# Optimization experiments

Hardware: AMD Instinct MI355X
Metric: run time of the kernel (lower is better)

## Reference

```python
import jax, jax.numpy as jnp
import numpy as np

D = 768          # wav2vec2-base hidden size
H = 4            # cross-attn heads
HD = D // H
B = 8
N = 1024         # w2v sequence length (target length)
T = 2000         # raw CQCC frames
N_GAT = 3
NUM_CLASSES = 2


def _p(key, shape, scale=0.02):
    return jax.random.normal(key, shape, dtype=jnp.float32) * scale


def layer_norm(x, g, b, eps=1e-5):
    m = x.mean(-1, keepdims=True)
    v = x.var(-1, keepdims=True)
    return (x - m) * jax.lax.rsqrt(v + eps) * g + b


def gelu(x):
    return jax.nn.gelu(x, approximate=False)


def conv1d(x, w, b):
    # x [B,C,T], w [O,I,K], padding=1 (same)
    y = jax.lax.conv_general_dilated(x, w, (1,), [(1, 1)], dimension_numbers=('NCH', 'OIH', 'NCH'))
    return y + b[None, :, None]


def batchnorm(x, g, b, m, v, eps=1e-5):
    # eval-mode BatchNorm1d on [B,C,T]
    return (x - m[None, :, None]) * jax.lax.rsqrt(v[None, :, None] + eps) * g[None, :, None] + b[None, :, None]


def interp_linear(x, target_len):
    # torch F.interpolate(mode='linear', align_corners=False); x [B,T,D] -> [B,target_len,D]
    t_in = x.shape[1]
    pos = (jnp.arange(target_len, dtype=jnp.float32) + 0.5) * (t_in / target_len) - 0.5
    pos = jnp.clip(pos, 0.0, t_in - 1.0)
    lo = jnp.floor(pos).astype(jnp.int32)
    hi = jnp.minimum(lo + 1, t_in - 1)
    w = (pos - lo.astype(jnp.float32))[None, :, None]
    return x[:, lo] * (1.0 - w) + x[:, hi] * w


def mha(q, k, v, in_w, in_b, out_w, out_b):
    # torch nn.MultiheadAttention, batch_first=True
    bb, nq, _ = q.shape
    nk = k.shape[1]
    wq, wk, wv = in_w[:D], in_w[D:2 * D], in_w[2 * D:]
    bq, bk, bv = in_b[:D], in_b[D:2 * D], in_b[2 * D:]
    qh = (q @ wq.T + bq).reshape(bb, nq, H, HD).transpose(0, 2, 1, 3)
    kh = (k @ wk.T + bk).reshape(bb, nk, H, HD).transpose(0, 2, 1, 3)
    vh = (v @ wv.T + bv).reshape(bb, nk, H, HD).transpose(0, 2, 1, 3)
    scores = jnp.einsum('bhqd,bhkd->bhqk', qh, kh) * (1.0 / np.sqrt(HD))
    alpha = jax.nn.softmax(scores, axis=-1)
    o = jnp.einsum('bhqk,bhkd->bhqd', alpha, vh).transpose(0, 2, 1, 3).reshape(bb, nq, D)
    return o @ out_w.T + out_b


def graph_attn(x, fc_w, fc_b, a_w, a_b):
    # GAT score on concat([h_i, h_j]) decomposes additively: e_ij = a_i.h_i + a_j.h_j + b
    h = x @ fc_w.T + fc_b                      # [B,N,D]
    s_i = h @ a_w[:D]                          # [B,N]
    s_j = h @ a_w[D:]                          # [B,N]
    e = s_i[:, :, None] + s_j[:, None, :] + a_b  # [B,N,N]
    alpha = jax.nn.softmax(e, axis=-1)
    return jnp.einsum('bij,bjd->bid', alpha, h)


def _forward(w2v, cqcc, conv1_w, conv1_b, bn1_g, bn1_b, bn1_m, bn1_v,
             conv2_w, conv2_b, bn2_g, bn2_b, bn2_m, bn2_v, pos_embed,
             lnq_g, lnq_b, lnkv_g, lnkv_b,
             a1_in_w, a1_in_b, a1_out_w, a1_out_b,
             a2_in_w, a2_in_b, a2_out_w, a2_out_b,
             gat_fc_w, gat_fc_b, gat_a_w, gat_a_b, gln_g, gln_b,
             clf_w1, clf_b1, clf_w2, clf_b2):
    # CQCC conv stack
    x = gelu(batchnorm(conv1d(cqcc, conv1_w, conv1_b), bn1_g, bn1_b, bn1_m, bn1_v))
    x = gelu(batchnorm(conv1d(x, conv2_w, conv2_b), bn2_g, bn2_b, bn2_m, bn2_v))  # [B,D,T]
    cq = interp_linear(x.transpose(0, 2, 1), w2v.shape[1])  # [B,N,D]
    # shared positional encoding
    n = w2v.shape[1]
    w = w2v + pos_embed[:, :n]
    cq = cq + pos_embed[:, :n]
    # bidirectional cross attention (norm_q / norm_kv shared across directions)
    out1 = mha(layer_norm(cq, lnq_g, lnq_b), layer_norm(w, lnkv_g, lnkv_b),
               layer_norm(w, lnkv_g, lnkv_b), a1_in_w, a1_in_b, a1_out_w, a1_out_b)
    out2 = mha(layer_norm(w, lnq_g, lnq_b), layer_norm(cq, lnkv_g, lnkv_b),
               layer_norm(cq, lnkv_g, lnkv_b), a2_in_w, a2_in_b, a2_out_w, a2_out_b)
    x = out1 + out2
    # 3 residual graph-attention blocks
    for l in range(N_GAT):
        res = x
        x = graph_attn(x, gat_fc_w[l], gat_fc_b[l], gat_a_w[l], gat_a_b[l])
        x = layer_norm(x + res, gln_g[l], gln_b[l])
    pooled = x.mean(axis=1)
    h = gelu(pooled @ clf_w1.T + clf_b1)
    return h @ clf_w2.T + clf_b2


def setup_inputs():
    ks = iter(jax.random.split(jax.random.key(0), 64))
    inp = {}
    inp['w2v'] = jax.random.normal(next(ks), (B, N, D), dtype=jnp.float32)
    inp['cqcc'] = jax.random.normal(next(ks), (B, 20, T), dtype=jnp.float32)
    inp['conv1_w'] = _p(next(ks), (128, 20, 3)); inp['conv1_b'] = jnp.zeros((128,), jnp.float32)
    inp['bn1_g'] = jnp.ones((128,), jnp.float32); inp['bn1_b'] = jnp.zeros((128,), jnp.float32)
    inp['bn1_m'] = jnp.zeros((128,), jnp.float32); inp['bn1_v'] = jnp.ones((128,), jnp.float32)
    inp['conv2_w'] = _p(next(ks), (D, 128, 3)); inp['conv2_b'] = jnp.zeros((D,), jnp.float32)
    inp['bn2_g'] = jnp.ones((D,), jnp.float32); inp['bn2_b'] = jnp.zeros((D,), jnp.float32)
    inp['bn2_m'] = jnp.zeros((D,), jnp.float32); inp['bn2_v'] = jnp.ones((D,), jnp.float32)
    inp['pos_embed'] = _p(next(ks), (1, 2000, D), 1.0)
    inp['lnq_g'] = jnp.ones((D,), jnp.float32); inp['lnq_b'] = jnp.zeros((D,), jnp.float32)
    inp['lnkv_g'] = jnp.ones((D,), jnp.float32); inp['lnkv_b'] = jnp.zeros((D,), jnp.float32)
    inp['a1_in_w'] = _p(next(ks), (3 * D, D)); inp['a1_in_b'] = jnp.zeros((3 * D,), jnp.float32)
    inp['a1_out_w'] = _p(next(ks), (D, D)); inp['a1_out_b'] = jnp.zeros((D,), jnp.float32)
    inp['a2_in_w'] = _p(next(ks), (3 * D, D)); inp['a2_in_b'] = jnp.zeros((3 * D,), jnp.float32)
    inp['a2_out_w'] = _p(next(ks), (D, D)); inp['a2_out_b'] = jnp.zeros((D,), jnp.float32)
    inp['gat_fc_w'] = _p(next(ks), (N_GAT, D, D)); inp['gat_fc_b'] = jnp.zeros((N_GAT, D), jnp.float32)
    inp['gat_a_w'] = _p(next(ks), (N_GAT, 2 * D)); inp['gat_a_b'] = jnp.zeros((N_GAT,), jnp.float32)
    inp['gln_g'] = jnp.ones((N_GAT, D), jnp.float32); inp['gln_b'] = jnp.zeros((N_GAT, D), jnp.float32)
    inp['clf_w1'] = _p(next(ks), (128, D)); inp['clf_b1'] = jnp.zeros((128,), jnp.float32)
    inp['clf_w2'] = _p(next(ks), (NUM_CLASSES, 128)); inp['clf_b2'] = jnp.zeros((NUM_CLASSES,), jnp.float32)
    return inp


def reference(w2v, cqcc, conv1_w, conv1_b, bn1_g, bn1_b, bn1_m, bn1_v,
              conv2_w, conv2_b, bn2_g, bn2_b, bn2_m, bn2_v, pos_embed,
              lnq_g, lnq_b, lnkv_g, lnkv_b,
              a1_in_w, a1_in_b, a1_out_w, a1_out_b,
              a2_in_w, a2_in_b, a2_out_w, a2_out_b,
              gat_fc_w, gat_fc_b, gat_a_w, gat_a_b, gln_g, gln_b,
              clf_w1, clf_b1, clf_w2, clf_b2):
    return _forward(w2v, cqcc, conv1_w, conv1_b, bn1_g, bn1_b, bn1_m, bn1_v,
                    conv2_w, conv2_b, bn2_g, bn2_b, bn2_m, bn2_v, pos_embed,
                    lnq_g, lnq_b, lnkv_g, lnkv_b,
                    a1_in_w, a1_in_b, a1_out_w, a1_out_b,
                    a2_in_w, a2_in_b, a2_out_w, a2_out_b,
                    gat_fc_w, gat_fc_b, gat_a_w, gat_a_b, gln_g, gln_b,
                    clf_w1, clf_b1, clf_w2, clf_b2)
```

## Files before the change

### kernel.cpp

```cpp
#include <hip/hip_runtime.h>
#include <math.h>

#define DD 768
#define NH 4
#define HDIM 192
#define BBATCH 8
#define NSEQ 1024
#define TLEN 2000
#define SLOT 6291456

typedef _Float16 h16;
typedef _Float16 half8v __attribute__((ext_vector_type(8)));
typedef _Float16 half4v __attribute__((ext_vector_type(4)));
typedef float f32x4 __attribute__((ext_vector_type(4)));

__device__ __forceinline__ float gelu_f(float x){
  return 0.5f * x * (1.0f + erff(x * 0.70710678118654752440f));
}
__device__ __forceinline__ float wave_sum(float v){
  #pragma unroll
  for (int off = 32; off; off >>= 1) v += __shfl_xor(v, off);
  return v;
}
__device__ __forceinline__ float wave_max(float v){
  #pragma unroll
  for (int off = 32; off; off >>= 1) v = fmaxf(v, __shfl_xor(v, off));
  return v;
}
__device__ __forceinline__ void gload16(const h16* g, h16* l){
  __builtin_amdgcn_global_load_lds(
      (const __attribute__((address_space(1))) void*)g,
      (__attribute__((address_space(3))) void*)l, 16, 0, 0);
}
__device__ __forceinline__ int xcd_remap(int orig, int nwg){
  int q = nwg >> 3, r = nwg & 7;
  int xcd = orig & 7, idx = orig >> 3;
  return (xcd < r ? xcd * (q + 1) : r * (q + 1) + (xcd - r) * q) + idx;
}

__global__ __launch_bounds__(256) void k_cast(const float* __restrict__ s,
    h16* __restrict__ d, int n){
  int i = blockIdx.x * 256 + threadIdx.x;
  if (i < n) d[i] = (h16)s[i];
}

__global__ __launch_bounds__(256) void k_conv1t(const float* __restrict__ cqcc,
    const float* __restrict__ w, const float* __restrict__ bias,
    const float* __restrict__ g, const float* __restrict__ be,
    const float* __restrict__ mm, const float* __restrict__ vv,
    float* __restrict__ out){
  __shared__ float xs[20][258];
  __shared__ float wsm[32*60];
  const int t0 = blockIdx.x * 256;
  const int ocg = blockIdx.y, b = blockIdx.z;
  const int tid = threadIdx.x;
  for (int idx = tid; idx < 20*258; idx += 256){
    int ic = idx / 258, tt = idx % 258;
    int t = t0 + tt - 1;
    xs[ic][tt] = (t >= 0 && t < TLEN) ? cqcc[((size_t)b*20 + ic)*TLEN + t] : 0.f;
  }
  for (int idx = tid; idx < 32*60; idx += 256)
    wsm[idx] = w[ocg*32*60 + idx];
  __syncthreads();
  int t = t0 + tid;
  if (t >= TLEN) return;
  float acc[32] = {};
  for (int ic = 0; ic < 20; ++ic){
    float x0 = xs[ic][tid], x1v = xs[ic][tid+1], x2v = xs[ic][tid+2];
    #pragma unroll
    for (int oc = 0; oc < 32; ++oc){
      const float* wp = &wsm[(oc*20 + ic)*3];
      acc[oc] += wp[0]*x0 + wp[1]*x1v + wp[2]*x2v;
    }
  }
  #pragma unroll 4
  for (int oc = 0; oc < 32; ++oc){
    int c = ocg*32 + oc;
    float s = rsqrtf(vv[c] + 1e-5f) * g[c];
    float val = (acc[oc] + bias[c] - mm[c]) * s + be[c];
    out[((size_t)b*128 + c)*TLEN + t] = gelu_f(val);
  }
}

__global__ __launch_bounds__(256) void k_im2col(const float* __restrict__ x1,
    h16* __restrict__ A2){
  int idx = blockIdx.x * 256 + threadIdx.x;
  if (idx >= 16000*384) return;
  int c = idx % 384, m = idx / 384;
  int b = m / TLEN, t = m % TLEN;
  int ic = c / 3, kh = c % 3;
  int ts = t + kh - 1;
  float v = (ts < 0 || ts >= TLEN) ? 0.f : x1[((size_t)b*128 + ic)*TLEN + ts];
  A2[idx] = (h16)v;
}

__global__ void k_bnprep(const float* __restrict__ cb, const float* __restrict__ g,
    const float* __restrict__ be, const float* __restrict__ m,
    const float* __restrict__ v, float* __restrict__ sc, float* __restrict__ off){
  int i = blockIdx.x * 256 + threadIdx.x;
  if (i >= DD) return;
  float s = g[i] * rsqrtf(v[i] + 1e-5f);
  sc[i] = s;
  off[i] = (cb[i] - m[i]) * s + be[i];
}

__global__ __launch_bounds__(256) void k_interp_ln(const float* __restrict__ x2,
    const float* __restrict__ pe,
    const float* __restrict__ g1, const float* __restrict__ b1, h16* __restrict__ o1,
    const float* __restrict__ g2, const float* __restrict__ b2, h16* __restrict__ o2){
  __shared__ float ss[4], sqq[4];
  int row = blockIdx.x, tid = threadIdx.x;
  int b = row >> 10, i = row & 1023;
  float p = (i + 0.5f) * ((float)TLEN / (float)NSEQ) - 0.5f;
  p = fminf(fmaxf(p, 0.f), (float)(TLEN - 1));
  int lo = (int)floorf(p);
  int hi = min(lo + 1, TLEN - 1);
  float w = p - (float)lo;
  const float* blo = x2 + ((size_t)b * TLEN + lo) * DD;
  const float* bhi = x2 + ((size_t)b * TLEN + hi) * DD;
  const float* per = pe + (size_t)i * DD;
  float v[3]; float s = 0.f, sq = 0.f;
  #pragma unroll
  for (int j = 0; j < 3; ++j){
    int d = j * 256 + tid;
    float x = blo[d] * (1.f - w) + bhi[d] * w + per[d];
    v[j] = x; s += x; sq += x * x;
  }
  s = wave_sum(s); sq = wave_sum(sq);
  int wv = tid >> 6;
  if ((tid & 63) == 0){ ss[wv] = s; sqq[wv] = sq; }
  __syncthreads();
  s  = ss[0] + ss[1] + ss[2] + ss[3];
  sq = sqq[0] + sqq[1] + sqq[2] + sqq[3];
  float mean = s * (1.f / DD);
  float var  = sq * (1.f / DD) - mean * mean;
  float r = rsqrtf(var + 1e-5f);
  #pragma unroll
  for (int j = 0; j < 3; ++j){
    int d = j * 256 + tid;
    float xn = (v[j] - mean) * r;
    o1[(size_t)row * DD + d] = (h16)(xn * g1[d] + b1[d]);
    o2[(size_t)row * DD + d] = (h16)(xn * g2[d] + b2[d]);
  }
}

__global__ __launch_bounds__(256) void k_addpos_ln(const float* __restrict__ xin,
    const float* __restrict__ pe,
    const float* __restrict__ g1, const float* __restrict__ b1, h16* __restrict__ o1,
    const float* __restrict__ g2, const float* __restrict__ b2, h16* __restrict__ o2){
  __shared__ float ss[4], sqq[4];
  int row = blockIdx.x, tid = threadIdx.x;
  int i = row & 1023;
  const float* ip = xin + (size_t)row * DD;
  const float* per = pe + (size_t)i * DD;
  float v[3]; float s = 0.f, sq = 0.f;
  #pragma unroll
  for (int j = 0; j < 3; ++j){
    int d = j * 256 + tid;
    float x = ip[d] + per[d];
    v[j] = x; s += x; sq += x * x;
  }
  s = wave_sum(s); sq = wave_sum(sq);
  int wv = tid >> 6;
  if ((tid & 63) == 0){ ss[wv] = s; sqq[wv] = sq; }
  __syncthreads();
  s  = ss[0] + ss[1] + ss[2] + ss[3];
  sq = sqq[0] + sqq[1] + sqq[2] + sqq[3];
  float mean = s * (1.f / DD);
  float var  = sq * (1.f / DD) - mean * mean;
  float r = rsqrtf(var + 1e-5f);
  #pragma unroll
  for (int j = 0; j < 3; ++j){
    int d = j * 256 + tid;
    float xn = (v[j] - mean) * r;
    o1[(size_t)row * DD + d] = (h16)(xn * g1[d] + b1[d]);
    o2[(size_t)row * DD + d] = (h16)(xn * g2[d] + b2[d]);
  }
}

__global__ __launch_bounds__(256) void k_ln2(const float* __restrict__ in,
    const float* __restrict__ ctx, const float* __restrict__ g,
    const float* __restrict__ be, float* __restrict__ outf, h16* __restrict__ outh){
  __shared__ float ss[4], sqq[4];
  int row = blockIdx.x, tid = threadIdx.x;
  const float* ip = in + (size_t)row * DD;
  int b = row >> 10;
  float v[3]; float s = 0.f, sq = 0.f;
  #pragma unroll
  for (int j = 0; j < 3; ++j){
    int d = j * 256 + tid;
    float x = ip[d];
    if (ctx) x += ctx[b * DD + d];
    v[j] = x; s += x; sq += x * x;
  }
  s = wave_sum(s); sq = wave_sum(sq);
  int w = tid >> 6;
  if ((tid & 63) == 0){ ss[w] = s; sqq[w] = sq; }
  __syncthreads();
  s  = ss[0] + ss[1] + ss[2] + ss[3];
  sq = sqq[0] + sqq[1] + sqq[2] + sqq[3];
  float mean = s * (1.f / DD);
  float var  = sq * (1.f / DD) - mean * mean;
  float r = rsqrtf(var + 1e-5f);
  #pragma unroll
  for (int j = 0; j < 3; ++j){
    int d = j * 256 + tid;
    float y = (v[j] - mean) * r * g[d] + be[d];
    if (outf) outf[(size_t)row * DD + d] = y;
    if (outh) outh[(size_t)row * DD + d] = (h16)y;
  }
}

#define GEMM_MAINLOOP(Abase, lda, Wbase, ldw, Kdim)                          \
  auto stage = [&](int buf, int kt){                                         \
    _Pragma("unroll")                                                        \
    for (int i = 0; i < 4; ++i){                                             \
      int p = i*256 + tid; int row = p >> 3; int ch = (p & 7) ^ (row & 7);   \
      gload16(Abase + (size_t)(m0+row)*lda + kt + ch*8, &Als[buf][p*8]);     \
    }                                                                        \
    _Pragma("unroll")                                                        \
    for (int i = 0; i < 4; ++i){                                             \
      int p = i*256 + tid; int row = p >> 3; int ch = (p & 7) ^ (row & 7);   \
      gload16(Wbase + (size_t)(n0+row)*ldw + kt + ch*8, &Bls[buf][p*8]);     \
    }                                                                        \
  };                                                                         \
  stage(0, 0);                                                               \
  const int nk = Kdim >> 6;                                                  \
  for (int t = 0; t < nk; ++t){                                              \
    const int cur = t & 1;                                                   \
    if (t + 1 < nk){                                                         \
      stage(cur ^ 1, (t + 1) << 6);                                          \
      asm volatile("s_waitcnt vmcnt(8)" ::: "memory");                       \
    } else {                                                                 \
      asm volatile("s_waitcnt vmcnt(0)" ::: "memory");                       \
    }                                                                        \
    __builtin_amdgcn_s_barrier();                                            \
    __builtin_amdgcn_sched_barrier(0);                                       \
    __builtin_amdgcn_s_setprio(1);                                           \
    _Pragma("unroll")                                                        \
    for (int kk = 0; kk < 2; ++kk){                                          \
      half8v af[4], bf[4];                                                   \
      _Pragma("unroll")                                                      \
      for (int mi = 0; mi < 4; ++mi){                                        \
        int row = wr*64 + mi*16 + lr;                                        \
        int chp = (kk*4 + lg) ^ (row & 7);                                   \
        af[mi] = *(const half8v*)&Als[cur][row*64 + chp*8];                  \
      }                                                                      \
      _Pragma("unroll")                                                      \
      for (int ni = 0; ni < 4; ++ni){                                        \
        int row = wc*64 + ni*16 + lr;                                        \
        int chp = (kk*4 + lg) ^ (row & 7);                                   \
        bf[ni] = *(const half8v*)&Bls[cur][row*64 + chp*8];                  \
      }                                                                      \
      _Pragma("unroll")                                                      \
      for (int mi = 0; mi < 4; ++mi)                                         \
        _Pragma("unroll")                                                    \
        for (int ni = 0; ni < 4; ++ni)                                       \
          acc[mi][ni] = __builtin_amdgcn_mfma_f32_16x16x32_f16(              \
              af[mi], bf[ni], acc[mi][ni], 0, 0, 0);                         \
    }                                                                        \
    __builtin_amdgcn_s_setprio(0);                                           \
    asm volatile("s_waitcnt lgkmcnt(0)" ::: "memory");                       \
    __builtin_amdgcn_sched_barrier(0);                                       \
    __builtin_amdgcn_s_barrier();                                            \
  }

__global__ __launch_bounds__(256) void k_gemm_h(
    const h16* __restrict__ A, const h16* __restrict__ W,
    int lda, int ldw, int ldc, int K,
    const float* __restrict__ bias, const float* __restrict__ sc,
    const float* __restrict__ off, const h16* __restrict__ addh,
    float* __restrict__ outf, h16* __restrict__ outh)
{
  __shared__ h16 Als[2][128*64];
  __shared__ h16 Bls[2][128*64];
  const int tid = threadIdx.x;
  const int gx = gridDim.x, gy = gridDim.y;
  const int wg = xcd_remap(blockIdx.x + gx * blockIdx.y, gx * gy);
  const int n0 = (wg % gx) * 128, m0 = (wg / gx) * 128;
  const int lane = tid & 63, wid = tid >> 6;
  const int wr = wid >> 1, wc = wid & 1;
  const int lr = lane & 15, lg = lane >> 4;
  f32x4 acc[4][4] = {};
  GEMM_MAINLOOP(A, lda, W, ldw, K)
  #pragma unroll
  for (int mi = 0; mi < 4; ++mi){
    #pragma unroll
    for (int ni = 0; ni < 4; ++ni){
      int col = n0 + wc*64 + ni*16 + lr;
      int rowb = m0 + wr*64 + mi*16 + lg*4;
      float cb = bias ? bias[col] : 0.f;
      #pragma unroll
      for (int r = 0; r < 4; ++r){
        size_t idx = (size_t)(rowb + r) * ldc + col;
        float v = acc[mi][ni][r];
        if (sc){ v = v * sc[col] + off[col]; v = gelu_f(v); }
        else v += cb;
        if (addh) v += (float)addh[idx];
        if (outf) outf[idx] = v;
        if (outh) outh[idx] = (h16)v;
      }
    }
  }
}

__global__ __launch_bounds__(256) void k_gemm6(
    const h16* __restrict__ Lall, const h16* __restrict__ w6,
    const float* __restrict__ b1, const float* __restrict__ b2,
    h16* __restrict__ qkv6)
{
  __shared__ h16 Als[2][128*64];
  __shared__ h16 Bls[2][128*64];
  const int tid = threadIdx.x;
  const int gx = gridDim.x, gy = gridDim.y;
  const int nwg = gx * gy * 6;
  const int wg = xcd_remap(blockIdx.x + gx*(blockIdx.y + gy*blockIdx.z), nwg);
  const int n0 = (wg % gx) * 128;
  const int m0 = ((wg / gx) % gy) * 128;
  const int bz = wg / (gx * gy);
  const int aidx = (1468 >> (2*bz)) & 3;
  const h16* A = Lall + (size_t)aidx * SLOT;
  const h16* W = w6 + (size_t)bz * 589824;
  const float* bias = (bz < 3 ? b1 + bz*DD : b2 + (bz-3)*DD);
  h16* C = qkv6 + (size_t)bz * SLOT;
  const int lane = tid & 63, wid = tid >> 6;
  const int wr = wid >> 1, wc = wid & 1;
  const int lr = lane & 15, lg = lane >> 4;
  f32x4 acc[4][4] = {};
  GEMM_MAINLOOP(A, DD, W, DD, DD)
  #pragma unroll
  for (int mi = 0; mi < 4; ++mi){
    #pragma unroll
    for (int ni = 0; ni < 4; ++ni){
      int col = n0 + wc*64 + ni*16 + lr;
      int rowb = m0 + wr*64 + mi*16 + lg*4;
      float cb = bias[col];
      #pragma unroll
      for (int r = 0; r < 4; ++r)
        C[(size_t)(rowb + r) * DD + col] = (h16)(acc[mi][ni][r] + cb);
    }
  }
}

__global__ __launch_bounds__(256) void k_trV(const h16* __restrict__ Vh, int ldv,
    h16* __restrict__ VT){
  __shared__ h16 tile[32][36];
  const int z = blockIdx.z, b = z >> 2, h = z & 3;
  const int q0 = blockIdx.x * 32, d0 = blockIdx.y * 32;
  const int t = threadIdx.x;
  {
    int qq = t >> 3, dg = (t & 7) * 4;
    const h16* src = Vh + ((size_t)b*NSEQ + q0 + qq)*ldv + h*HDIM + d0 + dg;
    half4v v = *(const half4v*)src;
    *(half4v*)&tile[qq][dg] = v;
  }
  __syncthreads();
  {
    int dd = t >> 3, qg = (t & 7) * 4;
    half4v ov;
    ov[0] = tile[qg+0][dd]; ov[1] = tile[qg+1][dd];
    ov[2] = tile[qg+2][dd]; ov[3] = tile[qg+3][dd];
    *(half4v*)(VT + (size_t)z*HDIM*NSEQ + (size_t)(d0+dd)*NSEQ + q0 + qg) = ov;
  }
}

__global__ __launch_bounds__(256) void k_flash(const h16* __restrict__ Qp,
    const h16* __restrict__ Kp, const h16* __restrict__ VTp,
    h16* __restrict__ Op){
  __shared__ h16 Ks[2][32*192];
  __shared__ h16 Vs[2][192*32];
  __shared__ h16 Ps[4][16*32];
  const int tid = threadIdx.x;
  const int bh = blockIdx.x, qt = blockIdx.y;
  const int b = bh >> 2, h = bh & 3;
  const int q0 = qt * 64;
  const h16* Qg = Qp + (size_t)b*NSEQ*DD + h*HDIM;
  const h16* Kg = Kp + (size_t)b*NSEQ*DD + h*HDIM;
  const h16* Vg = VTp + (size_t)bh*HDIM*NSEQ;
  const int lane = tid & 63, wid = tid >> 6;
  const int lr = lane & 15, lg = lane >> 4;
  half8v qf[6];
  {
    int qrow = q0 + wid*16 + lr;
    #pragma unroll
    for (int ks = 0; ks < 6; ++ks)
      qf[ks] = *(const half8v*)(Qg + (size_t)qrow*DD + ks*32 + lg*8);
  }
  auto stageK = [&](int buf, int k0){
    #pragma unroll
    for (int i = 0; i < 3; ++i){
      int p = i*256 + tid;
      int row = p / 24, chp = p % 24;
      int ch = chp ^ (row & 7);
      gload16(Kg + (size_t)(k0+row)*DD + ch*8, &Ks[buf][p*8]);
    }
  };
  auto stageV = [&](int buf, int k0){
    #pragma unroll
    for (int i = 0; i < 3; ++i){
      int p = i*256 + tid;
      int row = p >> 2, chp = p & 3;
      int ch = chp ^ ((row >> 1) & 3);
      gload16(Vg + (size_t)row*NSEQ + k0 + ch*8, &Vs[buf][p*8]);
    }
  };
  stageK(0, 0); stageV(0, 0);
  f32x4 oacc[12] = {};
  float m_run[4] = {-1e30f, -1e30f, -1e30f, -1e30f};
  float l_run[4] = {};
  const float SC = 0.07216878364870322f;
  __syncthreads();
  for (int kt = 0; kt < 32; ++kt){
    const int cur = kt & 1;
    if (kt + 1 < 32){ stageK(cur^1, (kt+1)*32); stageV(cur^1, (kt+1)*32); }
    f32x4 sacc[2] = {};
    __builtin_amdgcn_s_setprio(1);
    #pragma unroll
    for (int ks = 0; ks < 6; ++ks){
      #pragma unroll
      for (int t = 0; t < 2; ++t){
        int krow = t*16 + lr;
        int ch = (ks*4 + lg) ^ (krow & 7);
        half8v kf = *(const half8v*)&Ks[cur][krow*192 + ch*8];
        sacc[t] = __builtin_amdgcn_mfma_f32_16x16x32_f16(qf[ks], kf, sacc[t], 0, 0, 0);
      }
    }
    __builtin_amdgcn_s_setprio(0);
    float mnew[4], c[4], psum[4];
    #pragma unroll
    for (int r = 0; r < 4; ++r){
      float mt = fmaxf(sacc[0][r], sacc[1][r]);
      #pragma unroll
      for (int off = 1; off < 16; off <<= 1) mt = fmaxf(mt, __shfl_xor(mt, off));
      mnew[r] = fmaxf(m_run[r], mt * SC);
      c[r] = __expf(m_run[r] - mnew[r]);
      psum[r] = 0.f;
    }
    #pragma unroll
    for (int t = 0; t < 2; ++t){
      #pragma unroll
      for (int r = 0; r < 4; ++r){
        float p = __expf(sacc[t][r] * SC - mnew[r]);
        psum[r] += p;
        int q = lg*4 + r, key = t*16 + lr;
        int ch = (t*2 + (lr>>3)) ^ ((q>>1) & 3);
        Ps[wid][q*32 + ch*8 + (key & 7)] = (h16)p;
      }
    }
    #pragma unroll
    for (int r = 0; r < 4; ++r){
      #pragma unroll
      for (int off = 1; off < 16; off <<= 1) psum[r] += __shfl_xor(psum[r], off);
      l_run[r] = l_run[r] * c[r] + psum[r];
      m_run[r] = mnew[r];
    }
    #pragma unroll
    for (int dt = 0; dt < 12; ++dt){
      f32x4 o = oacc[dt];
      o[0] *= c[0]; o[1] *= c[1]; o[2] *= c[2]; o[3] *= c[3];
      oacc[dt] = o;
    }
    asm volatile("s_waitcnt lgkmcnt(0)" ::: "memory");
    __builtin_amdgcn_sched_barrier(0);
    {
      int pch = lg ^ ((lr >> 1) & 3);
      half8v pf = *(const half8v*)&Ps[wid][lr*32 + pch*8];
      __builtin_amdgcn_s_setprio(1);
      #pragma unroll
      for (int dt = 0; dt < 12; ++dt){
        int drow = dt*16 + lr;
        int vch = lg ^ ((drow >> 1) & 3);
        half8v vf = *(const half8v*)&Vs[cur][drow*32 + vch*8];
        oacc[dt] = __builtin_amdgcn_mfma_f32_16x16x32_f16(pf, vf, oacc[dt], 0, 0, 0);
      }
      __builtin_amdgcn_s_setprio(0);
    }
    __syncthreads();
  }
  float inv[4];
  #pragma unroll
  for (int r = 0; r < 4; ++r) inv[r] = 1.0f / l_run[r];
  h16* Og = Op + (size_t)b*NSEQ*DD + h*HDIM;
  #pragma unroll
  for (int dt = 0; dt < 12; ++dt){
    #pragma unroll
    for (int r = 0; r < 4; ++r){
      int q = q0 + wid*16 + lg*4 + r;
      Og[(size_t)q*DD + dt*16 + lr] = (h16)(oacc[dt][r] * inv[r]);
    }
  }
}

__global__ __launch_bounds__(128) void k_rowdot(const h16* __restrict__ h,
    const float* __restrict__ aw, float* __restrict__ sj){
  __shared__ float red[2];
  int row = blockIdx.x, tid = threadIdx.x;
  float s = 0.f;
  if (tid < 96){
    half8v v = *(const half8v*)(h + (size_t)row * DD + tid*8);
    #pragma unroll
    for (int j = 0; j < 8; ++j) s += (float)v[j] * aw[tid*8 + j];
  }
  s = wave_sum(s);
  if ((tid & 63) == 0) red[tid >> 6] = s;
  __syncthreads();
  if (tid == 0) sj[row] = red[0] + red[1];
}

__global__ __launch_bounds__(256) void k_softmax1024(const float* __restrict__ x,
    float* __restrict__ y){
  __shared__ float red[4];
  int b = blockIdx.x, tid = threadIdx.x;
  const float* ip = x + b * NSEQ;
  float v[4]; float mx = -1e30f;
  #pragma unroll
  for (int j = 0; j < 4; ++j){ v[j] = ip[j * 256 + tid]; mx = fmaxf(mx, v[j]); }
  mx = wave_max(mx);
  if ((tid & 63) == 0) red[tid >> 6] = mx;
  __syncthreads();
  mx = fmaxf(fmaxf(red[0], red[1]), fmaxf(red[2], red[3]));
  __syncthreads();
  float s = 0.f;
  #pragma unroll
  for (int j = 0; j < 4; ++j){ v[j] = __expf(v[j] - mx); s += v[j]; }
  s = wave_sum(s);
  if ((tid & 63) == 0) red[tid >> 6] = s;
  __syncthreads();
  s = red[0] + red[1] + red[2] + red[3];
  float inv = 1.0f / s;
  #pragma unroll
  for (int j = 0; j < 4; ++j) y[b * NSEQ + j * 256 + tid] = v[j] * inv;
}

__global__ __launch_bounds__(256) void k_ctx1(const float* __restrict__ alpha,
    const h16* __restrict__ h, float* __restrict__ part){
  int d = blockIdx.x * 256 + threadIdx.x;
  int b = blockIdx.y, pc = blockIdx.z;
  if (d >= DD) return;
  float acc = 0.f;
  const h16* hp = h + ((size_t)b * NSEQ + pc * 64) * DD + d;
  const float* ap = alpha + b * NSEQ + pc * 64;
  #pragma unroll 4
  for (int j = 0; j < 64; ++j) acc += ap[j] * (float)hp[(size_t)j * DD];
  part[(size_t)(b * 16 + pc) * DD + d] = acc;
}
__global__ __launch_bounds__(256) void k_ctx2(const float* __restrict__ part,
    float scale, float* __restrict__ ctx){
  int d = blockIdx.x * 256 + threadIdx.x;
  int b = blockIdx.y;
  if (d >= DD) return;
  float acc = 0.f;
  #pragma unroll
  for (int p = 0; p < 16; ++p) acc += part[(size_t)(b * 16 + p) * DD + d];
  ctx[b * DD + d] = acc * scale;
}

__global__ __launch_bounds__(256) void k_pool1(const float* __restrict__ x,
    float* __restrict__ part){
  int d = blockIdx.x * 256 + threadIdx.x;
  int b = blockIdx.y, pc = blockIdx.z;
  if (d >= DD) return;
  float acc = 0.f;
  const float* xp = x + ((size_t)b * NSEQ + pc * 64) * DD + d;
  #pragma unroll 4
  for (int j = 0; j < 64; ++j) acc += xp[(size_t)j * DD];
  part[(size_t)(b * 16 + pc) * DD + d] = acc;
}

__global__ __launch_bounds__(128) void k_clf(const float* __restrict__ pooled,
    const float* __restrict__ w1, const float* __restrict__ b1,
    const float* __restrict__ w2, const float* __restrict__ b2,
    float* __restrict__ out){
  __shared__ float pl[DD];
  __shared__ float h1[128];
  int b = blockIdx.x, tid = threadIdx.x;
  #pragma unroll
  for (int j = 0; j < 6; ++j) pl[j * 128 + tid] = pooled[b * DD + j * 128 + tid];
  __syncthreads();
  float acc = b1[tid];
  const float* wp = w1 + (size_t)tid * DD;
  for (int d = 0; d < DD; ++d) acc += pl[d] * wp[d];
  h1[tid] = gelu_f(acc);
  __syncthreads();
  if (tid < 2){
    float o = b2[tid];
    const float* w2p = w2 + tid * 128;
    for (int c = 0; c < 128; ++c) o += h1[c] * w2p[c];
    out[b * 2 + tid] = o;
  }
}

extern "C" void kernel_launch(void* const* d_in, const int* in_sizes, int n_in,
                              void* d_out, int out_size, void* d_ws, size_t ws_size,
                              hipStream_t stream){
  (void)in_sizes; (void)n_in; (void)out_size;
  const float* w2v      = (const float*)d_in[0];
  const float* cqcc     = (const float*)d_in[1];
  const float* conv1_w  = (const float*)d_in[2];
  const float* conv1_b  = (const float*)d_in[3];
  const float* bn1_g    = (const float*)d_in[4];
  const float* bn1_b    = (const float*)d_in[5];
  const float* bn1_m    = (const float*)d_in[6];
  const float* bn1_v    = (const float*)d_in[7];
  const float* conv2_w  = (const float*)d_in[8];
  const float* conv2_b  = (const float*)d_in[9];
  const float* bn2_g    = (const float*)d_in[10];
  const float* bn2_b    = (const float*)d_in[11];
  const float* bn2_m    = (const float*)d_in[12];
  const float* bn2_v    = (const float*)d_in[13];
  const float* pos_embed= (const float*)d_in[14];
  const float* lnq_g    = (const float*)d_in[15];
  const float* lnq_b    = (const float*)d_in[16];
  const float* lnkv_g   = (const float*)d_in[17];
  const float* lnkv_b   = (const float*)d_in[18];
  const float* a1_in_w  = (const float*)d_in[19];
  const float* a1_in_b  = (const float*)d_in[20];
  const float* a1_out_w = (const float*)d_in[21];
  const float* a1_out_b = (const float*)d_in[22];
  const float* a2_in_w  = (const float*)d_in[23];
  const float* a2_in_b  = (const float*)d_in[24];
  const float* a2_out_w = (const float*)d_in[25];
  const float* a2_out_b = (const float*)d_in[26];
  const float* gat_fc_w = (const float*)d_in[27];
  const float* gat_fc_b = (const float*)d_in[28];
  const float* gat_a_w  = (const float*)d_in[29];
  const float* gln_g    = (const float*)d_in[31];
  const float* gln_b    = (const float*)d_in[32];
  const float* clf_w1   = (const float*)d_in[33];
  const float* clf_b1   = (const float*)d_in[34];
  const float* clf_w2   = (const float*)d_in[35];
  const float* clf_b2   = (const float*)d_in[36];

  char* wsp = (char*)d_ws;
  auto F = [&](size_t bytes){ char* p = wsp; wsp += (bytes + 255) & ~(size_t)255; return p; };
  float* Abuf  = (float*)F(25165824);
  float* Bbuf  = (float*)F(25165824);
  h16* Lall    = (h16*)F(4*12582912);
  h16* qkv6    = (h16*)F(6*12582912);
  h16* VT      = (h16*)F(12582912);
  h16* o1h     = (h16*)F(12582912);
  h16* w6      = (h16*)F(2*3538944);
  h16* w_a1out = (h16*)F(1179648);
  h16* w_a2out = (h16*)F(1179648);
  h16* w_gat   = (h16*)F(3538944);
  h16* w_c2    = (h16*)F(589824);
  float* scb   = (float*)F(3072);
  float* offb  = (float*)F(3072);
  float* sj    = (float*)F(32768);
  float* alpha = (float*)F(32768);
  float* ctxb  = (float*)F(24576);
  float* pooled= (float*)F(24576);
  float* partb = (float*)F(393216);
  if ((size_t)(wsp - (char*)d_ws) > ws_size) return;

  float* x1  = (float*)Lall;
  h16*   A2  = Lall + 2*SLOT;
  float* x2f = (float*)qkv6;
  float* xb  = Abuf;
  h16*   xh  = (h16*)Bbuf;
  h16*   hh  = qkv6;

  const int NR = BBATCH * NSEQ;

  k_cast<<<(1769472+255)/256, 256, 0, stream>>>(a1_in_w,  w6,           1769472);
  k_cast<<<(1769472+255)/256, 256, 0, stream>>>(a2_in_w,  w6 + 1769472, 1769472);
  k_cast<<<(589824+255)/256,  256, 0, stream>>>(a1_out_w, w_a1out, 589824);
  k_cast<<<(589824+255)/256,  256, 0, stream>>>(a2_out_w, w_a2out, 589824);
  k_cast<<<(1769472+255)/256, 256, 0, stream>>>(gat_fc_w, w_gat,   1769472);
  k_cast<<<(294912+255)/256,  256, 0, stream>>>(conv2_w,  w_c2,    294912);
  k_bnprep<<<3, 256, 0, stream>>>(conv2_b, bn2_g, bn2_b, bn2_m, bn2_v, scb, offb);

  k_conv1t<<<dim3(8, 4, BBATCH), 256, 0, stream>>>(cqcc, conv1_w, conv1_b,
      bn1_g, bn1_b, bn1_m, bn1_v, x1);
  k_im2col<<<(16000*384+255)/256, 256, 0, stream>>>(x1, A2);
  k_gemm_h<<<dim3(6, 125), 256, 0, stream>>>(A2, w_c2, 384, 384, DD, 384,
      nullptr, scb, offb, nullptr, x2f, nullptr);

  k_interp_ln<<<NR, 256, 0, stream>>>(x2f, pos_embed,
      lnq_g, lnq_b, Lall, lnkv_g, lnkv_b, Lall + SLOT);
  k_addpos_ln<<<NR, 256, 0, stream>>>(w2v, pos_embed,
      lnq_g, lnq_b, Lall + 2*SLOT, lnkv_g, lnkv_b, Lall + 3*SLOT);

  k_gemm6<<<dim3(6, 64, 6), 256, 0, stream>>>(Lall, w6, a1_in_b, a2_in_b, qkv6);

  dim3 gflash(32, 16);

  k_trV<<<dim3(32, 6, 32), 256, 0, stream>>>(qkv6 + 2*(size_t)SLOT, DD, VT);
  k_flash<<<gflash, 256, 0, stream>>>(qkv6, qkv6 + (size_t)SLOT, VT, qkv6);
  k_gemm_h<<<dim3(6, 64), 256, 0, stream>>>(qkv6, w_a1out, DD, DD, DD, DD,
      a1_out_b, nullptr, nullptr, nullptr, nullptr, o1h);

  k_trV<<<dim3(32, 6, 32), 256, 0, stream>>>(qkv6 + 5*(size_t)SLOT, DD, VT);
  k_flash<<<gflash, 256, 0, stream>>>(qkv6 + 3*(size_t)SLOT, qkv6 + 4*(size_t)SLOT,
                                      VT, qkv6 + 3*(size_t)SLOT);
  k_gemm_h<<<dim3(6, 64), 256, 0, stream>>>(qkv6 + 3*(size_t)SLOT, w_a2out,
      DD, DD, DD, DD, a2_out_b, nullptr, nullptr, o1h, xb, xh);

  for (int l = 0; l < 3; ++l){
    k_gemm_h<<<dim3(6, 64), 256, 0, stream>>>(xh, w_gat + (size_t)l*589824,
        DD, DD, DD, DD, gat_fc_b + l*DD, nullptr, nullptr, nullptr, nullptr, hh);
    k_rowdot<<<NR, 128, 0, stream>>>(hh, gat_a_w + l*2*DD + DD, sj);
    k_softmax1024<<<BBATCH, 256, 0, stream>>>(sj, alpha);
    k_ctx1<<<dim3(3, BBATCH, 16), 256, 0, stream>>>(alpha, hh, partb);
    k_ctx2<<<dim3(3, BBATCH), 256, 0, stream>>>(partb, 1.0f, ctxb);
    k_ln2<<<NR, 256, 0, stream>>>(xb, ctxb, gln_g + l*DD, gln_b + l*DD, xb, xh);
  }

  k_pool1<<<dim3(3, BBATCH, 16), 256, 0, stream>>>(xb, partb);
  k_ctx2<<<dim3(3, BBATCH), 256, 0, stream>>>(partb, 1.0f/NSEQ, pooled);
  k_clf<<<BBATCH, 128, 0, stream>>>(pooled, clf_w1, clf_b1, clf_w2, clf_b2,
                                    (float*)d_out);
}
```

Measured before the change: 644.5 us.

## Fuse GAT row-dot into GEMM epilogue, store residuals in fp16, widen V transpose

The GAT scoring row-dot is computed in the GEMM epilogue as per-tile partial sums, and the softmax kernel now reduces those 12 partials per row. This removes the separate rowdot kernel and its reread of h. The conv2 output and the residual stream x are now kept only in fp16, cutting fp32 traffic in interp, LN and pooling. The V transpose uses 64x64 swizzled tiles with 16-byte accesses. The residual path in half precision may lose accuracy.

```diff
diff --git a/kernel.cpp b/kernel.cpp
--- a/kernel.cpp
+++ b/kernel.cpp
@@ -104,7 +104,7 @@
   off[i] = (cb[i] - m[i]) * s + be[i];
 }
 
-__global__ __launch_bounds__(256) void k_interp_ln(const float* __restrict__ x2,
+__global__ __launch_bounds__(256) void k_interp_ln(const h16* __restrict__ x2,
     const float* __restrict__ pe,
     const float* __restrict__ g1, const float* __restrict__ b1, h16* __restrict__ o1,
     const float* __restrict__ g2, const float* __restrict__ b2, h16* __restrict__ o2){
@@ -116,14 +116,14 @@
   int lo = (int)floorf(p);
   int hi = min(lo + 1, TLEN - 1);
   float w = p - (float)lo;
-  const float* blo = x2 + ((size_t)b * TLEN + lo) * DD;
-  const float* bhi = x2 + ((size_t)b * TLEN + hi) * DD;
+  const h16* blo = x2 + ((size_t)b * TLEN + lo) * DD;
+  const h16* bhi = x2 + ((size_t)b * TLEN + hi) * DD;
   const float* per = pe + (size_t)i * DD;
   float v[3]; float s = 0.f, sq = 0.f;
   #pragma unroll
   for (int j = 0; j < 3; ++j){
     int d = j * 256 + tid;
-    float x = blo[d] * (1.f - w) + bhi[d] * w + per[d];
+    float x = (float)blo[d] * (1.f - w) + (float)bhi[d] * w + per[d];
     v[j] = x; s += x; sq += x * x;
   }
   s = wave_sum(s); sq = wave_sum(sq);
@@ -178,19 +178,18 @@
   }
 }
 
-__global__ __launch_bounds__(256) void k_ln2(const float* __restrict__ in,
+__global__ __launch_bounds__(256) void k_lnH(const h16* __restrict__ in,
     const float* __restrict__ ctx, const float* __restrict__ g,
-    const float* __restrict__ be, float* __restrict__ outf, h16* __restrict__ outh){
+    const float* __restrict__ be, h16* __restrict__ out){
   __shared__ float ss[4], sqq[4];
   int row = blockIdx.x, tid = threadIdx.x;
-  const float* ip = in + (size_t)row * DD;
+  const h16* ip = in + (size_t)row * DD;
   int b = row >> 10;
   float v[3]; float s = 0.f, sq = 0.f;
   #pragma unroll
   for (int j = 0; j < 3; ++j){
     int d = j * 256 + tid;
-    float x = ip[d];
-    if (ctx) x += ctx[b * DD + d];
+    float x = (float)ip[d] + ctx[b * DD + d];
     v[j] = x; s += x; sq += x * x;
   }
   s = wave_sum(s); sq = wave_sum(sq);
@@ -205,9 +204,7 @@
   #pragma unroll
   for (int j = 0; j < 3; ++j){
     int d = j * 256 + tid;
-    float y = (v[j] - mean) * r * g[d] + be[d];
-    if (outf) outf[(size_t)row * DD + d] = y;
-    if (outh) outh[(size_t)row * DD + d] = (h16)y;
+    out[(size_t)row * DD + d] = (h16)((v[j] - mean) * r * g[d] + be[d]);
   }
 }
 
@@ -270,19 +267,22 @@
     int lda, int ldw, int ldc, int K,
     const float* __restrict__ bias, const float* __restrict__ sc,
     const float* __restrict__ off, const h16* __restrict__ addh,
-    float* __restrict__ outf, h16* __restrict__ outh)
+    float* __restrict__ outf, h16* __restrict__ outh,
+    const float* __restrict__ rdw, float* __restrict__ rdpart)
 {
   __shared__ h16 Als[2][128*64];
   __shared__ h16 Bls[2][128*64];
   const int tid = threadIdx.x;
   const int gx = gridDim.x, gy = gridDim.y;
   const int wg = xcd_remap(blockIdx.x + gx * blockIdx.y, gx * gy);
-  const int n0 = (wg % gx) * 128, m0 = (wg / gx) * 128;
+  const int nidx = wg % gx;
+  const int n0 = nidx * 128, m0 = (wg / gx) * 128;
   const int lane = tid & 63, wid = tid >> 6;
   const int wr = wid >> 1, wc = wid & 1;
   const int lr = lane & 15, lg = lane >> 4;
   f32x4 acc[4][4] = {};
   GEMM_MAINLOOP(A, lda, W, ldw, K)
+  float rd[4][4] = {};
   #pragma unroll
   for (int mi = 0; mi < 4; ++mi){
     #pragma unroll
@@ -290,6 +290,7 @@
       int col = n0 + wc*64 + ni*16 + lr;
       int rowb = m0 + wr*64 + mi*16 + lg*4;
       float cb = bias ? bias[col] : 0.f;
+      float aw = rdw ? rdw[col] : 0.f;
       #pragma unroll
       for (int r = 0; r < 4; ++r){
         size_t idx = (size_t)(rowb + r) * ldc + col;
@@ -299,6 +300,22 @@
         if (addh) v += (float)addh[idx];
         if (outf) outf[idx] = v;
         if (outh) outh[idx] = (h16)v;
+        if (rdw) rd[mi][r] += v * aw;
+      }
+    }
+  }
+  if (rdw){
+    #pragma unroll
+    for (int mi = 0; mi < 4; ++mi){
+      #pragma unroll
+      for (int r = 0; r < 4; ++r){
+        float p = rd[mi][r];
+        #pragma unroll
+        for (int o = 1; o < 16; o <<= 1) p += __shfl_xor(p, o);
+        if (lr == 0){
+          int row = m0 + wr*64 + mi*16 + lg*4 + r;
+          rdpart[(size_t)row * 12 + nidx*2 + wc] = p;
+        }
       }
     }
   }
@@ -344,23 +361,32 @@
 
 __global__ __launch_bounds__(256) void k_trV(const h16* __restrict__ Vh, int ldv,
     h16* __restrict__ VT){
-  __shared__ h16 tile[32][36];
+  __shared__ h16 tile[64*64];
   const int z = blockIdx.z, b = z >> 2, h = z & 3;
-  const int q0 = blockIdx.x * 32, d0 = blockIdx.y * 32;
+  const int q0 = blockIdx.x * 64, d0 = blockIdx.y * 64;
   const int t = threadIdx.x;
   {
-    int qq = t >> 3, dg = (t & 7) * 4;
-    const h16* src = Vh + ((size_t)b*NSEQ + q0 + qq)*ldv + h*HDIM + d0 + dg;
-    half4v v = *(const half4v*)src;
-    *(half4v*)&tile[qq][dg] = v;
+    int qq = t >> 2, ds = (t & 3) * 16;
+    const h16* src = Vh + ((size_t)b*NSEQ + q0 + qq)*ldv + h*HDIM + d0 + ds;
+    half8v v0 = *(const half8v*)src;
+    half8v v1 = *(const half8v*)(src + 8);
+    int c0 = (ds >> 3) ^ (qq & 7), c1 = ((ds >> 3) + 1) ^ (qq & 7);
+    *(half8v*)&tile[qq*64 + c0*8] = v0;
+    *(half8v*)&tile[qq*64 + c1*8] = v1;
   }
   __syncthreads();
   {
-    int dd = t >> 3, qg = (t & 7) * 4;
-    half4v ov;
-    ov[0] = tile[qg+0][dd]; ov[1] = tile[qg+1][dd];
-    ov[2] = tile[qg+2][dd]; ov[3] = tile[qg+3][dd];
-    *(half4v*)(VT + (size_t)z*HDIM*NSEQ + (size_t)(d0+dd)*NSEQ + q0 + qg) = ov;
+    int dd = t >> 2, qs = (t & 3) * 16;
+    half8v o0, o1;
+    #pragma unroll
+    for (int j = 0; j < 8; ++j){
+      int q = qs + j, q2 = qs + 8 + j;
+      o0[j] = tile[q*64  + (((dd>>3) ^ (q&7))*8)  + (dd & 7)];
+      o1[j] = tile[q2*64 + (((dd>>3) ^ (q2&7))*8) + (dd & 7)];
+    }
+    h16* dst = VT + (size_t)z*HDIM*NSEQ + (size_t)(d0+dd)*NSEQ + q0 + qs;
+    *(half8v*)dst = o0;
+    *(half8v*)(dst + 8) = o1;
   }
 }
 
@@ -491,30 +517,20 @@
   }
 }
 
-__global__ __launch_bounds__(128) void k_rowdot(const h16* __restrict__ h,
-    const float* __restrict__ aw, float* __restrict__ sj){
-  __shared__ float red[2];
-  int row = blockIdx.x, tid = threadIdx.x;
-  float s = 0.f;
-  if (tid < 96){
-    half8v v = *(const half8v*)(h + (size_t)row * DD + tid*8);
-    #pragma unroll
-    for (int j = 0; j < 8; ++j) s += (float)v[j] * aw[tid*8 + j];
-  }
-  s = wave_sum(s);
-  if ((tid & 63) == 0) red[tid >> 6] = s;
-  __syncthreads();
-  if (tid == 0) sj[row] = red[0] + red[1];
-}
-
-__global__ __launch_bounds__(256) void k_softmax1024(const float* __restrict__ x,
+__global__ __launch_bounds__(256) void k_softmax12(const float* __restrict__ part,
     float* __restrict__ y){
   __shared__ float red[4];
   int b = blockIdx.x, tid = threadIdx.x;
-  const float* ip = x + b * NSEQ;
   float v[4]; float mx = -1e30f;
   #pragma unroll
-  for (int j = 0; j < 4; ++j){ v[j] = ip[j * 256 + tid]; mx = fmaxf(mx, v[j]); }
+  for (int j = 0; j < 4; ++j){
+    int i = j * 256 + tid;
+    const float* p = part + (size_t)(b * NSEQ + i) * 12;
+    float s = 0.f;
+    #pragma unroll
+    for (int k = 0; k < 12; ++k) s += p[k];
+    v[j] = s; mx = fmaxf(mx, s);
+  }
   mx = wave_max(mx);
   if ((tid & 63) == 0) red[tid >> 6] = mx;
   __syncthreads();
@@ -555,15 +571,15 @@
   ctx[b * DD + d] = acc * scale;
 }
 
-__global__ __launch_bounds__(256) void k_pool1(const float* __restrict__ x,
+__global__ __launch_bounds__(256) void k_pool1(const h16* __restrict__ x,
     float* __restrict__ part){
   int d = blockIdx.x * 256 + threadIdx.x;
   int b = blockIdx.y, pc = blockIdx.z;
   if (d >= DD) return;
   float acc = 0.f;
-  const float* xp = x + ((size_t)b * NSEQ + pc * 64) * DD + d;
+  const h16* xp = x + ((size_t)b * NSEQ + pc * 64) * DD + d;
   #pragma unroll 4
-  for (int j = 0; j < 64; ++j) acc += xp[(size_t)j * DD];
+  for (int j = 0; j < 64; ++j) acc += (float)xp[(size_t)j * DD];
   part[(size_t)(b * 16 + pc) * DD + d] = acc;
 }
 
@@ -633,8 +649,7 @@
 
   char* wsp = (char*)d_ws;
   auto F = [&](size_t bytes){ char* p = wsp; wsp += (bytes + 255) & ~(size_t)255; return p; };
-  float* Abuf  = (float*)F(25165824);
-  float* Bbuf  = (float*)F(25165824);
+  h16* xh      = (h16*)F(12582912);
   h16* Lall    = (h16*)F(4*12582912);
   h16* qkv6    = (h16*)F(6*12582912);
   h16* VT      = (h16*)F(12582912);
@@ -646,7 +661,6 @@
   h16* w_c2    = (h16*)F(589824);
   float* scb   = (float*)F(3072);
   float* offb  = (float*)F(3072);
-  float* sj    = (float*)F(32768);
   float* alpha = (float*)F(32768);
   float* ctxb  = (float*)F(24576);
   float* pooled= (float*)F(24576);
@@ -655,9 +669,7 @@
 
   float* x1  = (float*)Lall;
   h16*   A2  = Lall + 2*SLOT;
-  float* x2f = (float*)qkv6;
-  float* xb  = Abuf;
-  h16*   xh  = (h16*)Bbuf;
+  h16*   x2h = qkv6;
   h16*   hh  = qkv6;
 
   const int NR = BBATCH * NSEQ;
@@ -674,9 +686,9 @@
       bn1_g, bn1_b, bn1_m, bn1_v, x1);
   k_im2col<<<(16000*384+255)/256, 256, 0, stream>>>(x1, A2);
   k_gemm_h<<<dim3(6, 125), 256, 0, stream>>>(A2, w_c2, 384, 384, DD, 384,
-      nullptr, scb, offb, nullptr, x2f, nullptr);
-
-  k_interp_ln<<<NR, 256, 0, stream>>>(x2f, pos_embed,
+      nullptr, scb, offb, nullptr, nullptr, x2h, nullptr, nullptr);
+
+  k_interp_ln<<<NR, 256, 0, stream>>>(x2h, pos_embed,
       lnq_g, lnq_b, Lall, lnkv_g, lnkv_b, Lall + SLOT);
   k_addpos_ln<<<NR, 256, 0, stream>>>(w2v, pos_embed,
       lnq_g, lnq_b, Lall + 2*SLOT, lnkv_g, lnkv_b, Lall + 3*SLOT);
@@ -685,28 +697,28 @@
 
   dim3 gflash(32, 16);
 
-  k_trV<<<dim3(32, 6, 32), 256, 0, stream>>>(qkv6 + 2*(size_t)SLOT, DD, VT);
+  k_trV<<<dim3(16, 3, 32), 256, 0, stream>>>(qkv6 + 2*(size_t)SLOT, DD, VT);
   k_flash<<<gflash, 256, 0, stream>>>(qkv6, qkv6 + (size_t)SLOT, VT, qkv6);
   k_gemm_h<<<dim3(6, 64), 256, 0, stream>>>(qkv6, w_a1out, DD, DD, DD, DD,
-      a1_out_b, nullptr, nullptr, nullptr, nullptr, o1h);
-
-  k_trV<<<dim3(32, 6, 32), 256, 0, stream>>>(qkv6 + 5*(size_t)SLOT, DD, VT);
+      a1_out_b, nullptr, nullptr, nullptr, nullptr, o1h, nullptr, nullptr);
+
+  k_trV<<<dim3(16, 3, 32), 256, 0, stream>>>(qkv6 + 5*(size_t)SLOT, DD, VT);
   k_flash<<<gflash, 256, 0, stream>>>(qkv6 + 3*(size_t)SLOT, qkv6 + 4*(size_t)SLOT,
                                       VT, qkv6 + 3*(size_t)SLOT);
   k_gemm_h<<<dim3(6, 64), 256, 0, stream>>>(qkv6 + 3*(size_t)SLOT, w_a2out,
-      DD, DD, DD, DD, a2_out_b, nullptr, nullptr, o1h, xb, xh);
+      DD, DD, DD, DD, a2_out_b, nullptr, nullptr, o1h, nullptr, xh, nullptr, nullptr);
 
   for (int l = 0; l < 3; ++l){
     k_gemm_h<<<dim3(6, 64), 256, 0, stream>>>(xh, w_gat + (size_t)l*589824,
-        DD, DD, DD, DD, gat_fc_b + l*DD, nullptr, nullptr, nullptr, nullptr, hh);
-    k_rowdot<<<NR, 128, 0, stream>>>(hh, gat_a_w + l*2*DD + DD, sj);
-    k_softmax1024<<<BBATCH, 256, 0, stream>>>(sj, alpha);
+        DD, DD, DD, DD, gat_fc_b + l*DD, nullptr, nullptr, nullptr,
+        nullptr, hh, gat_a_w + l*2*DD + DD, partb);
+    k_softmax12<<<BBATCH, 256, 0, stream>>>(partb, alpha);
     k_ctx1<<<dim3(3, BBATCH, 16), 256, 0, stream>>>(alpha, hh, partb);
     k_ctx2<<<dim3(3, BBATCH), 256, 0, stream>>>(partb, 1.0f, ctxb);
-    k_ln2<<<NR, 256, 0, stream>>>(xb, ctxb, gln_g + l*DD, gln_b + l*DD, xb, xh);
-  }
-
-  k_pool1<<<dim3(3, BBATCH, 16), 256, 0, stream>>>(xb, partb);
+    k_lnH<<<NR, 256, 0, stream>>>(xh, ctxb, gln_g + l*DD, gln_b + l*DD, xh);
+  }
+
+  k_pool1<<<dim3(3, BBATCH, 16), 256, 0, stream>>>(xh, partb);
   k_ctx2<<<dim3(3, BBATCH), 256, 0, stream>>>(partb, 1.0f/NSEQ, pooled);
   k_clf<<<BBATCH, 128, 0, stream>>>(pooled, clf_w1, clf_b1, clf_w2, clf_b2,
                                     (float*)d_out);
```

New measurement: 623.0 us. 1.03x faster.
